# Kernel tuning notes

Measured on AMD Instinct MI355X. Metric: run time of the kernel, lower is better.

The kernel has to match this reference:

```python
import jax, jax.numpy as jnp
import numpy as np

B, S, D, H = 2, 2048, 1024, 16
HD = D // H  # head_dim = 64


def setup_inputs() -> dict:
    key = jax.random.key(0)
    ks = jax.random.split(key, 5)
    scale = 1.0 / np.sqrt(D)  # xavier-ish init scale
    return {
        "x": jax.random.normal(ks[0], (B, S, D), jnp.float32),
        "Wq": jax.random.normal(ks[1], (D, D), jnp.float32) * scale,
        "Wk": jax.random.normal(ks[2], (D, D), jnp.float32) * scale,
        "Wv": jax.random.normal(ks[3], (D, D), jnp.float32) * scale,
        "Wo": jax.random.normal(ks[4], (D, D), jnp.float32) * scale,
        "bo": jnp.zeros((D,), jnp.float32),
    }


def reference(x, Wq, Wk, Wv, Wo, bo):
    # nn.Linear stores weight as [out, in]; y = x @ W.T
    b, s, d = x.shape
    def heads(t):
        return t.reshape(b, s, H, HD).transpose(0, 2, 1, 3)  # [B,H,S,HD]
    Q = heads(x @ Wq.T)
    K = heads(x @ Wk.T)
    V = heads(x @ Wv.T)
    # Chunked loop in the original sees all K per Q-chunk => full attention.
    scores = jnp.einsum("bhqd,bhkd->bhqk", Q, K) / np.sqrt(HD)
    attn = jax.nn.softmax(scores, axis=-1)
    out = jnp.einsum("bhqk,bhkd->bhqd", attn, V)
    out = out.transpose(0, 2, 1, 3).reshape(b, s, d)
    return out @ Wo.T + bo
```

## Files before the change

### kernel.cpp

```cpp
#include <hip/hip_runtime.h>
#include <hip/hip_bf16.h>
#include <math.h>

#define Bc 2
#define Sc 2048
#define Dc 1024
#define Hc 16
#define HDc 64
#define Mc (Bc*Sc)

using f32x4  = __attribute__((ext_vector_type(4))) float;
using bf16x8 = __attribute__((ext_vector_type(8))) short;
using s16x4  = __attribute__((ext_vector_type(4))) short;
using uint4v = __attribute__((ext_vector_type(4))) unsigned int;

#define GAS(p) ((const __attribute__((address_space(1))) void*)(p))
#define LAS(p) ((__attribute__((address_space(3))) void*)(p))

#define QSC 0.18033688011112042f

__device__ __forceinline__ short f2b(float f) {
  union { float f; unsigned u; } v; v.f = f;
  unsigned r = (v.u + 0x7fffu + ((v.u >> 16) & 1u)) >> 16;
  return (short)r;
}

__global__ __launch_bounds__(256) void cvt_all(
    const float* __restrict__ x,
    const float* __restrict__ Wq, const float* __restrict__ Wk,
    const float* __restrict__ Wv, const float* __restrict__ Wo,
    short* __restrict__ xb, short* __restrict__ wqb, short* __restrict__ wkb,
    short* __restrict__ wvb, short* __restrict__ wob) {
  int i = blockIdx.x * 256 + threadIdx.x;
  const float* in; short* out; int idx;
  if (i < (1 << 20)) {
    in = x; out = xb; idx = i;
  } else {
    int j = i - (1 << 20);
    int s = j >> 18; idx = j & 262143;
    in  = (s == 0) ? Wq  : (s == 1) ? Wk  : (s == 2) ? Wv  : Wo;
    out = (s == 0) ? wqb : (s == 1) ? wkb : (s == 2) ? wvb : wob;
  }
  float4 v = reinterpret_cast<const float4*>(in)[idx];
  s16x4 o;
  o.x = f2b(v.x); o.y = f2b(v.y); o.z = f2b(v.z); o.w = f2b(v.w);
  reinterpret_cast<s16x4*>(out)[idx] = o;
}

__device__ __forceinline__ void gemm_core_128(
    const short* __restrict__ A, const short* __restrict__ Bt,
    int m0, int n0, short* As, short* Bs, f32x4 (&acc)[4][4]) {
  const int tid = threadIdx.x;
  const int l = tid & 63;
  const int w = tid >> 6;
  const int wr = w >> 1, wc = w & 1;
  const int g = l >> 4;

  int srow[4], scol[4];
#pragma unroll
  for (int i = 0; i < 4; ++i) {
    int off = w * 1024 + i * 4096 + l * 16;
    int row = off >> 7;
    srow[i] = row;
    scol[i] = (off & 127) ^ ((row & 7) << 4);
  }
  const int rA = (wr * 64 + (l & 15)) * 128;
  const int rB = (wc * 64 + (l & 15)) * 128;
  const int sw = (l & 7) << 4;

  for (int kt = 0; kt < 16; ++kt) {
#pragma unroll
    for (int i = 0; i < 4; ++i) {
      const char* ga = (const char*)A + (size_t)(m0 + srow[i]) * 2048 + kt * 128 + scol[i];
      const char* gb = (const char*)Bt + (size_t)(n0 + srow[i]) * 2048 + kt * 128 + scol[i];
      __builtin_amdgcn_global_load_lds(GAS(ga), LAS((char*)As + w * 1024 + i * 4096), 16, 0, 0);
      __builtin_amdgcn_global_load_lds(GAS(gb), LAS((char*)Bs + w * 1024 + i * 4096), 16, 0, 0);
    }
    __syncthreads();
#pragma unroll
    for (int ks = 0; ks < 2; ++ks) {
      bf16x8 af[4], bfr[4];
#pragma unroll
      for (int mi = 0; mi < 4; ++mi)
        af[mi] = *(const bf16x8*)((const char*)As + rA + mi * 2048 + ((g * 16 + ks * 64) ^ sw));
#pragma unroll
      for (int ni = 0; ni < 4; ++ni)
        bfr[ni] = *(const bf16x8*)((const char*)Bs + rB + ni * 2048 + ((g * 16 + ks * 64) ^ sw));
#pragma unroll
      for (int mi = 0; mi < 4; ++mi)
#pragma unroll
        for (int ni = 0; ni < 4; ++ni)
          acc[mi][ni] = __builtin_amdgcn_mfma_f32_16x16x32_bf16(af[mi], bfr[ni], acc[mi][ni], 0, 0, 0);
    }
    __syncthreads();
  }
}

__global__ __launch_bounds__(256) void qkv_kernel(
    const short* __restrict__ xb, const short* __restrict__ wq,
    const short* __restrict__ wk, const short* __restrict__ wv,
    short* __restrict__ Qb, short* __restrict__ Kb, short* __restrict__ Vtg) {
  __shared__ short As[128 * 64];
  __shared__ short Bs[128 * 64];
  const int mt = blockIdx.x, yb = blockIdx.y;
  const int sel = yb >> 3, nb = yb & 7;
  const short* Wt = (sel == 0) ? wq : (sel == 1) ? wk : wv;
  f32x4 acc[4][4];
#pragma unroll
  for (int i = 0; i < 4; ++i)
#pragma unroll
    for (int j = 0; j < 4; ++j)
#pragma unroll
      for (int r = 0; r < 4; ++r) acc[i][j][r] = 0.0f;
  gemm_core_128(xb, Wt, mt * 128, nb * 128, As, Bs, acc);
  const int l = threadIdx.x & 63, w = threadIdx.x >> 6;
  const int wr = w >> 1, wc = w & 1, g = l >> 4, c = l & 15;

  if (sel == 2) {
#pragma unroll
    for (int mi = 0; mi < 4; ++mi)
#pragma unroll
      for (int ni = 0; ni < 4; ++ni) {
        int n = nb * 128 + wc * 64 + ni * 16 + c;
        int h = n >> 6, hd = n & 63;
        int m = mt * 128 + wr * 64 + mi * 16 + g * 4;
        int b = m >> 11, s = m & 2047;
        s16x4 pk;
#pragma unroll
        for (int r = 0; r < 4; ++r) pk[r] = f2b(acc[mi][ni][r]);
        *(s16x4*)(Vtg + ((size_t)(b * 16 + h) * 64 + hd) * 2048 + s) = pk;
      }
  } else {
    short* Ob = (sel == 0) ? Qb : Kb;
    const float oscale = (sel == 0) ? QSC : 1.0f;
#pragma unroll
    for (int mi = 0; mi < 4; ++mi)
#pragma unroll
      for (int ni = 0; ni < 4; ++ni) {
        int n = nb * 128 + wc * 64 + ni * 16 + c;
        int h = n >> 6, hd = n & 63;
#pragma unroll
        for (int r = 0; r < 4; ++r) {
          int m = mt * 128 + wr * 64 + mi * 16 + g * 4 + r;
          int b = m >> 11, s = m & 2047;
          Ob[((size_t)(b * 16 + h) * 2048 + s) * 64 + hd] = f2b(acc[mi][ni][r] * oscale);
        }
      }
  }
}

__global__ __launch_bounds__(256) void oproj_kernel(
    const short* __restrict__ ab, const short* __restrict__ wo,
    const float* __restrict__ bo, float* __restrict__ out) {
  __shared__ short As[128 * 64];
  __shared__ short Bs[128 * 64];
  const int mt = blockIdx.x, nb = blockIdx.y;
  f32x4 acc[4][4];
#pragma unroll
  for (int i = 0; i < 4; ++i)
#pragma unroll
    for (int j = 0; j < 4; ++j)
#pragma unroll
      for (int r = 0; r < 4; ++r) acc[i][j][r] = 0.0f;
  gemm_core_128(ab, wo, mt * 128, nb * 128, As, Bs, acc);
  const int l = threadIdx.x & 63, w = threadIdx.x >> 6;
  const int wr = w >> 1, wc = w & 1, g = l >> 4;
#pragma unroll
  for (int mi = 0; mi < 4; ++mi)
#pragma unroll
    for (int ni = 0; ni < 4; ++ni) {
      int n = nb * 128 + wc * 64 + ni * 16 + (l & 15);
      float bias = bo[n];
#pragma unroll
      for (int r = 0; r < 4; ++r) {
        int m = mt * 128 + wr * 64 + mi * 16 + g * 4 + r;
        out[(size_t)m * 1024 + n] = acc[mi][ni][r] + bias;
      }
    }
}

__global__ __launch_bounds__(512, 4) void attn_kernel(
    const short* __restrict__ Qb, const short* __restrict__ Kb,
    const short* __restrict__ Vtg, short* __restrict__ ab) {
  __shared__ char lds[49152];
  const int bh = blockIdx.x;
  const int qt = blockIdx.y;
  const int tid = threadIdx.x, l = tid & 63, w = tid >> 6;
  const int qg = w >> 1, h = w & 1;
  const int g = l >> 4, c = l & 15;
  const int sw = (l & 7) << 4;
  const bool godd = (l & 16) != 0;
  const short* Qp = Qb + (size_t)bh * Sc * HDc;
  const char* KpB = (const char*)(Kb + (size_t)bh * Sc * HDc);
  const char* VtB = (const char*)(Vtg + (size_t)bh * Sc * HDc);
  const int q0 = qt * 128 + qg * 32;

  bf16x8 bq[2][2];
#pragma unroll
  for (int qf = 0; qf < 2; ++qf)
#pragma unroll
    for (int ks = 0; ks < 2; ++ks)
      bq[qf][ks] = *(const bf16x8*)(Qp + (size_t)(q0 + qf * 16 + c) * 64 + ks * 32 + g * 8);

  f32x4 o[2][4];
  float lsum[2] = {0.0f, 0.0f};
#pragma unroll
  for (int qf = 0; qf < 2; ++qf)
#pragma unroll
    for (int ohf = 0; ohf < 4; ++ohf)
#pragma unroll
      for (int r = 0; r < 4; ++r) o[qf][ohf][r] = 0.0f;

  const int soff = w * 1024 + l * 16;
  const int srow = soff >> 7;
  const int scol = (soff & 127) ^ ((srow & 7) << 4);
  const size_t koff = (size_t)srow * 128 + scol;
  const size_t voff = (size_t)srow * 4096 + scol;
  const int ldst = w * 1024;

#define ISSUE3(t_) do {                                                               \
    char* kd_ = lds + ((t_) % 3) * 8192 + ldst;                                       \
    char* vd_ = lds + 24576 + ((t_) % 3) * 8192 + ldst;                               \
    __builtin_amdgcn_global_load_lds(GAS(KpB + (size_t)(t_) * 8192 + koff), LAS(kd_), 16, 0, 0); \
    __builtin_amdgcn_global_load_lds(GAS(VtB + (size_t)(t_) * 128  + voff), LAS(vd_), 16, 0, 0); \
  } while (0)

  ISSUE3(0);
  ISSUE3(1);

  for (int t = 0; t < 32; ++t) {
    if (t < 31) {
      asm volatile("s_waitcnt vmcnt(2)" ::: "memory");
    } else {
      asm volatile("s_waitcnt vmcnt(0)" ::: "memory");
    }
    __builtin_amdgcn_s_barrier();
    if (t < 30) ISSUE3(t + 2);

    const char* KsB = lds + (t % 3) * 8192;
    const char* VsB = lds + 24576 + (t % 3) * 8192;

    f32x4 s[2][2];
#pragma unroll
    for (int qf = 0; qf < 2; ++qf)
#pragma unroll
      for (int kf2 = 0; kf2 < 2; ++kf2)
#pragma unroll
        for (int r = 0; r < 4; ++r) s[qf][kf2][r] = 0.0f;
#pragma unroll
    for (int ks = 0; ks < 2; ++ks) {
      bf16x8 ak[2];
#pragma unroll
      for (int kf2 = 0; kf2 < 2; ++kf2) {
        int row = (2 * h + kf2) * 16 + c;
        ak[kf2] = *(const bf16x8*)(KsB + row * 128 + ((ks * 64 + g * 16) ^ sw));
      }
      __builtin_amdgcn_s_setprio(1);
#pragma unroll
      for (int qf = 0; qf < 2; ++qf)
#pragma unroll
        for (int kf2 = 0; kf2 < 2; ++kf2)
          s[qf][kf2] = __builtin_amdgcn_mfma_f32_16x16x32_bf16(ak[kf2], bq[qf][ks], s[qf][kf2], 0, 0, 0);
      __builtin_amdgcn_s_setprio(0);
    }

    bf16x8 pb[2];
#pragma unroll
    for (int qf = 0; qf < 2; ++qf) {
      float p[2][4];
#pragma unroll
      for (int kf2 = 0; kf2 < 2; ++kf2)
#pragma unroll
        for (int r = 0; r < 4; ++r)
          p[kf2][r] = __builtin_amdgcn_exp2f(s[qf][kf2][r]);
      float t0 = (p[0][0] + p[0][1]) + (p[0][2] + p[0][3]);
      float t1 = (p[1][0] + p[1][1]) + (p[1][2] + p[1][3]);
      lsum[qf] += t0 + t1;

      unsigned dw[2][2];
#pragma unroll
      for (int kf2 = 0; kf2 < 2; ++kf2)
#pragma unroll
        for (int d = 0; d < 2; ++d)
          asm("v_cvt_pk_bf16_f32 %0, %1, %2" : "=v"(dw[kf2][d]) : "v"(p[kf2][2 * d]), "v"(p[kf2][2 * d + 1]));

      unsigned T[4];
#pragma unroll
      for (int d = 0; d < 2; ++d) {
        unsigned Av = dw[0][d], Bv = dw[1][d];
        asm("v_permlane32_swap_b32 %0, %1" : "+v"(Av), "+v"(Bv));
        unsigned sAv = (unsigned)__shfl_xor((int)Av, 16);
        unsigned sBv = (unsigned)__shfl_xor((int)Bv, 16);
        T[d]     = godd ? sBv : Av;
        T[d + 2] = godd ? Bv  : sAv;
      }
      uint4v t4; t4.x = T[0]; t4.y = T[1]; t4.z = T[2]; t4.w = T[3];
      pb[qf] = __builtin_bit_cast(bf16x8, t4);
    }

    {
      bf16x8 av[4];
#pragma unroll
      for (int ohf = 0; ohf < 4; ++ohf) {
        int row = ohf * 16 + c;
        av[ohf] = *(const bf16x8*)(VsB + row * 128 + ((h * 64 + g * 16) ^ sw));
      }
      __builtin_amdgcn_s_setprio(1);
#pragma unroll
      for (int ohf = 0; ohf < 4; ++ohf) {
        o[0][ohf] = __builtin_amdgcn_mfma_f32_16x16x32_bf16(av[ohf], pb[0], o[0][ohf], 0, 0, 0);
        o[1][ohf] = __builtin_amdgcn_mfma_f32_16x16x32_bf16(av[ohf], pb[1], o[1][ohf], 0, 0, 0);
      }
      __builtin_amdgcn_s_setprio(0);
    }
  }

  float* So = (float*)lds;
  float* Sl = (float*)(lds + 24576);
  const int b = bh >> 4, hh = bh & 15;
  float lv[2];

  __syncthreads();
#pragma unroll
  for (int qf = 0; qf < 2; ++qf) {
    if (h == 1) {
#pragma unroll
      for (int ohf = 0; ohf < 4; ++ohf)
        *(f32x4*)(So + qg * 1024 + l * 16 + ohf * 4) = o[qf][ohf];
      if (qf == 0) {
        Sl[qg * 128 + l * 2 + 0] = lsum[0];
        Sl[qg * 128 + l * 2 + 1] = lsum[1];
      }
    }
    __syncthreads();
    if (h == 0) {
      if (qf == 0) {
#pragma unroll
        for (int j = 0; j < 2; ++j) {
          float lt = lsum[j] + Sl[qg * 128 + l * 2 + j];
          lt += __shfl_xor(lt, 16);
          lt += __shfl_xor(lt, 32);
          lv[j] = 1.0f / lt;
        }
      }
      int q = q0 + qf * 16 + c;
      short* dst = ab + (size_t)(b * Sc + q) * Dc + hh * 64 + g * 4;
#pragma unroll
      for (int ohf = 0; ohf < 4; ++ohf) {
        f32x4 om = o[qf][ohf] + *(const f32x4*)(So + qg * 1024 + l * 16 + ohf * 4);
        s16x4 pk4;
#pragma unroll
        for (int r = 0; r < 4; ++r) pk4[r] = f2b(om[r] * lv[qf]);
        *(s16x4*)(dst + ohf * 16) = pk4;
      }
    }
    __syncthreads();
  }
}

extern "C" void kernel_launch(void* const* d_in, const int* in_sizes, int n_in,
                              void* d_out, int out_size, void* d_ws, size_t ws_size,
                              hipStream_t stream) {
  const float* x  = (const float*)d_in[0];
  const float* Wq = (const float*)d_in[1];
  const float* Wk = (const float*)d_in[2];
  const float* Wv = (const float*)d_in[3];
  const float* Wo = (const float*)d_in[4];
  const float* bo = (const float*)d_in[5];
  float* out = (float*)d_out;

  char* p = (char*)d_ws;
  short* xb    = (short*)p; p += (size_t)Mc * Dc * 2;
  short* wqb   = (short*)p; p += (size_t)Dc * Dc * 2;
  short* wkb   = (short*)p; p += (size_t)Dc * Dc * 2;
  short* wvb   = (short*)p; p += (size_t)Dc * Dc * 2;
  short* wob   = (short*)p; p += (size_t)Dc * Dc * 2;
  short* Qb    = (short*)p; p += (size_t)Mc * Dc * 2;
  short* Kb    = (short*)p; p += (size_t)Mc * Dc * 2;
  short* Vtg   = (short*)p; p += (size_t)Mc * Dc * 2;
  short* attnb = (short*)p; p += (size_t)Mc * Dc * 2;

  cvt_all<<<8192, 256, 0, stream>>>(x, Wq, Wk, Wv, Wo, xb, wqb, wkb, wvb, wob);
  qkv_kernel<<<dim3(Mc / 128, 24), 256, 0, stream>>>(xb, wqb, wkb, wvb, Qb, Kb, Vtg);
  attn_kernel<<<dim3(Bc * Hc, Sc / 128), 512, 0, stream>>>(Qb, Kb, Vtg, attnb);
  oproj_kernel<<<dim3(Mc / 128, Dc / 128), 256, 0, stream>>>(attnb, wob, bo, out);
}
```

Measured before the change: 192.1 us.

## Halve attention query tile to 64 rows to double grid and raise occupancy

```diff
diff --git a/kernel.cpp b/kernel.cpp
--- a/kernel.cpp
+++ b/kernel.cpp
@@ -179,7 +179,7 @@
     }
 }
 
-__global__ __launch_bounds__(512, 4) void attn_kernel(
+__global__ __launch_bounds__(512, 6) void attn_kernel(
     const short* __restrict__ Qb, const short* __restrict__ Kb,
     const short* __restrict__ Vtg, short* __restrict__ ab) {
   __shared__ char lds[49152];
@@ -193,23 +193,19 @@
   const short* Qp = Qb + (size_t)bh * Sc * HDc;
   const char* KpB = (const char*)(Kb + (size_t)bh * Sc * HDc);
   const char* VtB = (const char*)(Vtg + (size_t)bh * Sc * HDc);
-  const int q0 = qt * 128 + qg * 32;
-
-  bf16x8 bq[2][2];
-#pragma unroll
-  for (int qf = 0; qf < 2; ++qf)
-#pragma unroll
-    for (int ks = 0; ks < 2; ++ks)
-      bq[qf][ks] = *(const bf16x8*)(Qp + (size_t)(q0 + qf * 16 + c) * 64 + ks * 32 + g * 8);
-
-  f32x4 o[2][4];
-  float lsum[2] = {0.0f, 0.0f};
-#pragma unroll
-  for (int qf = 0; qf < 2; ++qf)
-#pragma unroll
-    for (int ohf = 0; ohf < 4; ++ohf)
-#pragma unroll
-      for (int r = 0; r < 4; ++r) o[qf][ohf][r] = 0.0f;
+  const int q0 = qt * 64 + qg * 16;
+
+  bf16x8 bq[2];
+#pragma unroll
+  for (int ks = 0; ks < 2; ++ks)
+    bq[ks] = *(const bf16x8*)(Qp + (size_t)(q0 + c) * 64 + ks * 32 + g * 8);
+
+  f32x4 o[4];
+  float lsum = 0.0f;
+#pragma unroll
+  for (int ohf = 0; ohf < 4; ++ohf)
+#pragma unroll
+    for (int r = 0; r < 4; ++r) o[ohf][r] = 0.0f;
 
   const int soff = w * 1024 + l * 16;
   const int srow = soff >> 7;
@@ -240,13 +236,11 @@
     const char* KsB = lds + (t % 3) * 8192;
     const char* VsB = lds + 24576 + (t % 3) * 8192;
 
-    f32x4 s[2][2];
-#pragma unroll
-    for (int qf = 0; qf < 2; ++qf)
-#pragma unroll
-      for (int kf2 = 0; kf2 < 2; ++kf2)
-#pragma unroll
-        for (int r = 0; r < 4; ++r) s[qf][kf2][r] = 0.0f;
+    f32x4 s[2];
+#pragma unroll
+    for (int kf2 = 0; kf2 < 2; ++kf2)
+#pragma unroll
+      for (int r = 0; r < 4; ++r) s[kf2][r] = 0.0f;
 #pragma unroll
     for (int ks = 0; ks < 2; ++ks) {
       bf16x8 ak[2];
@@ -257,25 +251,22 @@
       }
       __builtin_amdgcn_s_setprio(1);
 #pragma unroll
-      for (int qf = 0; qf < 2; ++qf)
-#pragma unroll
-        for (int kf2 = 0; kf2 < 2; ++kf2)
-          s[qf][kf2] = __builtin_amdgcn_mfma_f32_16x16x32_bf16(ak[kf2], bq[qf][ks], s[qf][kf2], 0, 0, 0);
+      for (int kf2 = 0; kf2 < 2; ++kf2)
+        s[kf2] = __builtin_amdgcn_mfma_f32_16x16x32_bf16(ak[kf2], bq[ks], s[kf2], 0, 0, 0);
       __builtin_amdgcn_s_setprio(0);
     }
 
-    bf16x8 pb[2];
-#pragma unroll
-    for (int qf = 0; qf < 2; ++qf) {
+    bf16x8 pb;
+    {
       float p[2][4];
 #pragma unroll
       for (int kf2 = 0; kf2 < 2; ++kf2)
 #pragma unroll
         for (int r = 0; r < 4; ++r)
-          p[kf2][r] = __builtin_amdgcn_exp2f(s[qf][kf2][r]);
+          p[kf2][r] = __builtin_amdgcn_exp2f(s[kf2][r]);
       float t0 = (p[0][0] + p[0][1]) + (p[0][2] + p[0][3]);
       float t1 = (p[1][0] + p[1][1]) + (p[1][2] + p[1][3]);
-      lsum[qf] += t0 + t1;
+      lsum += t0 + t1;
 
       unsigned dw[2][2];
 #pragma unroll
@@ -295,7 +286,7 @@
         T[d + 2] = godd ? Bv  : sAv;
       }
       uint4v t4; t4.x = T[0]; t4.y = T[1]; t4.z = T[2]; t4.w = T[3];
-      pb[qf] = __builtin_bit_cast(bf16x8, t4);
+      pb = __builtin_bit_cast(bf16x8, t4);
     }
 
     {
@@ -307,54 +298,39 @@
       }
       __builtin_amdgcn_s_setprio(1);
 #pragma unroll
-      for (int ohf = 0; ohf < 4; ++ohf) {
-        o[0][ohf] = __builtin_amdgcn_mfma_f32_16x16x32_bf16(av[ohf], pb[0], o[0][ohf], 0, 0, 0);
-        o[1][ohf] = __builtin_amdgcn_mfma_f32_16x16x32_bf16(av[ohf], pb[1], o[1][ohf], 0, 0, 0);
-      }
+      for (int ohf = 0; ohf < 4; ++ohf)
+        o[ohf] = __builtin_amdgcn_mfma_f32_16x16x32_bf16(av[ohf], pb, o[ohf], 0, 0, 0);
       __builtin_amdgcn_s_setprio(0);
     }
   }
 
-  float* So = (float*)lds;
   float* Sl = (float*)(lds + 24576);
   const int b = bh >> 4, hh = bh & 15;
-  float lv[2];
 
   __syncthreads();
-#pragma unroll
-  for (int qf = 0; qf < 2; ++qf) {
-    if (h == 1) {
-#pragma unroll
-      for (int ohf = 0; ohf < 4; ++ohf)
-        *(f32x4*)(So + qg * 1024 + l * 16 + ohf * 4) = o[qf][ohf];
-      if (qf == 0) {
-        Sl[qg * 128 + l * 2 + 0] = lsum[0];
-        Sl[qg * 128 + l * 2 + 1] = lsum[1];
-      }
-    }
-    __syncthreads();
-    if (h == 0) {
-      if (qf == 0) {
-#pragma unroll
-        for (int j = 0; j < 2; ++j) {
-          float lt = lsum[j] + Sl[qg * 128 + l * 2 + j];
-          lt += __shfl_xor(lt, 16);
-          lt += __shfl_xor(lt, 32);
-          lv[j] = 1.0f / lt;
-        }
-      }
-      int q = q0 + qf * 16 + c;
-      short* dst = ab + (size_t)(b * Sc + q) * Dc + hh * 64 + g * 4;
-#pragma unroll
-      for (int ohf = 0; ohf < 4; ++ohf) {
-        f32x4 om = o[qf][ohf] + *(const f32x4*)(So + qg * 1024 + l * 16 + ohf * 4);
-        s16x4 pk4;
-#pragma unroll
-        for (int r = 0; r < 4; ++r) pk4[r] = f2b(om[r] * lv[qf]);
-        *(s16x4*)(dst + ohf * 16) = pk4;
-      }
-    }
-    __syncthreads();
+  if (h == 1) {
+#pragma unroll
+    for (int ohf = 0; ohf < 4; ++ohf)
+      *(f32x4*)(lds + qg * 4096 + ((l * 64 + ohf * 16) ^ ((l & 7) << 4))) = o[ohf];
+    Sl[qg * 64 + l] = lsum;
+  }
+  __syncthreads();
+  if (h == 0) {
+    float lt = lsum + Sl[qg * 64 + l];
+    lt += __shfl_xor(lt, 16);
+    lt += __shfl_xor(lt, 32);
+    float inv = 1.0f / lt;
+    int q = q0 + c;
+    short* dst = ab + (size_t)(b * Sc + q) * Dc + hh * 64 + g * 4;
+#pragma unroll
+    for (int ohf = 0; ohf < 4; ++ohf) {
+      f32x4 om = o[ohf] +
+          *(const f32x4*)(lds + qg * 4096 + ((l * 64 + ohf * 16) ^ ((l & 7) << 4)));
+      s16x4 pk4;
+#pragma unroll
+      for (int r = 0; r < 4; ++r) pk4[r] = f2b(om[r] * inv);
+      *(s16x4*)(dst + ohf * 16) = pk4;
+    }
   }
 }
 
@@ -382,6 +358,6 @@
 
   cvt_all<<<8192, 256, 0, stream>>>(x, Wq, Wk, Wv, Wo, xb, wqb, wkb, wvb, wob);
   qkv_kernel<<<dim3(Mc / 128, 24), 256, 0, stream>>>(xb, wqb, wkb, wvb, Qb, Kb, Vtg);
-  attn_kernel<<<dim3(Bc * Hc, Sc / 128), 512, 0, stream>>>(Qb, Kb, Vtg, attnb);
+  attn_kernel<<<dim3(Bc * Hc, Sc / 64), 512, 0, stream>>>(Qb, Kb, Vtg, attnb);
   oproj_kernel<<<dim3(Mc / 128, Dc / 128), 256, 0, stream>>>(attnb, wob, bo, out);
 }
```

Result: slower. 201.5 us (+4.9%).

## Rewrite QKV GEMM as 256x256 tile with pipelined async LDS loads

Applied to the files above, without the earlier changes.

```diff
diff --git a/kernel.cpp b/kernel.cpp
--- a/kernel.cpp
+++ b/kernel.cpp
@@ -18,6 +18,9 @@
 #define LAS(p) ((__attribute__((address_space(3))) void*)(p))
 
 #define QSC 0.18033688011112042f
+
+#define SCB __builtin_amdgcn_sched_barrier(0)
+#define BARR __builtin_amdgcn_s_barrier()
 
 __device__ __forceinline__ short f2b(float f) {
   union { float f; unsigned u; } v; v.f = f;
@@ -96,34 +99,137 @@
   }
 }
 
-__global__ __launch_bounds__(256) void qkv_kernel(
+__global__ __launch_bounds__(512, 2) void qkv_kernel(
     const short* __restrict__ xb, const short* __restrict__ wq,
     const short* __restrict__ wk, const short* __restrict__ wv,
     short* __restrict__ Qb, short* __restrict__ Kb, short* __restrict__ Vtg) {
-  __shared__ short As[128 * 64];
-  __shared__ short Bs[128 * 64];
-  const int mt = blockIdx.x, yb = blockIdx.y;
-  const int sel = yb >> 3, nb = yb & 7;
+  __shared__ char lds[131072];
+  const int tid = threadIdx.x, l = tid & 63, w = tid >> 6;
+  const int g = l >> 4, c = l & 15;
+  const int sw = (l & 7) << 4;
+  const int wm = w >> 2, wn = w & 3;
+  const int mt = blockIdx.x, nb = blockIdx.y;
+  const int sel = nb >> 2, nbq = nb & 3;
   const short* Wt = (sel == 0) ? wq : (sel == 1) ? wk : wv;
-  f32x4 acc[4][4];
-#pragma unroll
-  for (int i = 0; i < 4; ++i)
+  const char* Ag = (const char*)xb;
+  const char* Bg = (const char*)Wt;
+
+  const int la = (w & 3) * 64 + l;
+  const int lb = (w >> 2) * 64 + l;
+  const int arow0 = la >> 3;
+  const int acol  = ((la * 16) & 127) ^ ((arow0 & 7) << 4);
+  const int brow0 = lb >> 3;
+  const int bcol  = ((lb * 16) & 127) ^ ((brow0 & 7) << 4);
+
+#define STG_A(t_, hi_) do {                                                           \
+    char* d_ = lds + ((((t_) & 1) * 2 + wm) << 14) + (w & 3) * 1024 + (hi_) * 8192;   \
+    const char* s_ = Ag + (size_t)(mt * 256 + wm * 128 + (hi_) * 64 + arow0) * 2048   \
+                     + (t_) * 128 + acol;                                             \
+    __builtin_amdgcn_global_load_lds(GAS(s_), LAS(d_), 16, 0, 0);                     \
+    __builtin_amdgcn_global_load_lds(GAS(s_ + 32 * 2048), LAS(d_ + 4096), 16, 0, 0);  \
+  } while (0)
+
+#define STG_B(t_, hi_) do {                                                           \
+    char* d_ = lds + 65536 + ((t_) & 1) * 32768 + wn * 8192 + (w >> 2) * 1024         \
+               + (hi_) * 4096;                                                        \
+    const char* s_ = Bg + (size_t)(nbq * 256 + wn * 64 + (hi_) * 32 + brow0) * 2048   \
+                     + (t_) * 128 + bcol;                                             \
+    __builtin_amdgcn_global_load_lds(GAS(s_), LAS(d_), 16, 0, 0);                     \
+    __builtin_amdgcn_global_load_lds(GAS(s_ + 16 * 2048), LAS(d_ + 2048), 16, 0, 0);  \
+  } while (0)
+
+  f32x4 acc[8][4];
+#pragma unroll
+  for (int i = 0; i < 8; ++i)
 #pragma unroll
     for (int j = 0; j < 4; ++j)
 #pragma unroll
       for (int r = 0; r < 4; ++r) acc[i][j][r] = 0.0f;
-  gemm_core_128(xb, Wt, mt * 128, nb * 128, As, Bs, acc);
-  const int l = threadIdx.x & 63, w = threadIdx.x >> 6;
-  const int wr = w >> 1, wc = w & 1, g = l >> 4, c = l & 15;
+
+  bf16x8 a[4][2], blo[2][2], bhi[2][2];
+
+#define LD_A(mh_) do {                                                                \
+    _Pragma("unroll")                                                                 \
+    for (int mi2 = 0; mi2 < 4; ++mi2)                                                 \
+      _Pragma("unroll")                                                               \
+      for (int ks = 0; ks < 2; ++ks)                                                  \
+        a[mi2][ks] = *(const bf16x8*)(Ah + ((mh_) * 64 + mi2 * 16 + c) * 128 +        \
+                                      ((ks * 64 + g * 16) ^ sw));                     \
+  } while (0)
+
+#define LD_B(arr_, nh_) do {                                                          \
+    _Pragma("unroll")                                                                 \
+    for (int ni2 = 0; ni2 < 2; ++ni2)                                                 \
+      _Pragma("unroll")                                                               \
+      for (int ks = 0; ks < 2; ++ks)                                                  \
+        arr_[ni2][ks] = *(const bf16x8*)(Bq + ((nh_) * 32 + ni2 * 16 + c) * 128 +     \
+                                         ((ks * 64 + g * 16) ^ sw));                  \
+  } while (0)
+
+#define MMQ(mh_, arr_, nh_) do {                                                      \
+    __builtin_amdgcn_s_setprio(1);                                                    \
+    _Pragma("unroll")                                                                 \
+    for (int ks = 0; ks < 2; ++ks)                                                    \
+      _Pragma("unroll")                                                               \
+      for (int mi2 = 0; mi2 < 4; ++mi2)                                               \
+        _Pragma("unroll")                                                             \
+        for (int ni2 = 0; ni2 < 2; ++ni2)                                             \
+          acc[(mh_) * 4 + mi2][(nh_) * 2 + ni2] =                                     \
+              __builtin_amdgcn_mfma_f32_16x16x32_bf16(                                \
+                  a[mi2][ks], arr_[ni2][ks], acc[(mh_) * 4 + mi2][(nh_) * 2 + ni2],   \
+                  0, 0, 0);                                                           \
+    __builtin_amdgcn_s_setprio(0);                                                    \
+  } while (0)
+
+  STG_A(0, 0); STG_B(0, 0); STG_B(0, 1); STG_A(0, 1);
+  asm volatile("s_waitcnt vmcnt(4)" ::: "memory");
+  BARR; SCB;
+
+  for (int t = 0; t < 16; ++t) {
+    const int db = t & 1;
+    const char* Ah = lds + ((db * 2 + wm) << 14);
+    const char* Bq = lds + 65536 + db * 32768 + wn * 8192;
+    const bool st = t < 15;
+
+    LD_A(0); LD_B(blo, 0);
+    if (st) STG_A(t + 1, 0);
+    BARR; SCB;
+    MMQ(0, blo, 0);
+    if (st) asm volatile("s_waitcnt vmcnt(4)" ::: "memory");
+    else    asm volatile("s_waitcnt vmcnt(2)" ::: "memory");
+    BARR; SCB;
+
+    LD_B(bhi, 1);
+    if (st) STG_B(t + 1, 0);
+    BARR; SCB;
+    MMQ(0, bhi, 1);
+    if (st) asm volatile("s_waitcnt vmcnt(4)" ::: "memory");
+    else    asm volatile("s_waitcnt vmcnt(0)" ::: "memory");
+    BARR; SCB;
+
+    LD_A(1);
+    if (st) STG_B(t + 1, 1);
+    BARR; SCB;
+    MMQ(1, bhi, 1);
+    BARR; SCB;
+
+    if (st) STG_A(t + 1, 1);
+    BARR; SCB;
+    MMQ(1, blo, 0);
+    if (st) {
+      asm volatile("s_waitcnt vmcnt(4)" ::: "memory");
+      BARR; SCB;
+    }
+  }
 
   if (sel == 2) {
 #pragma unroll
-    for (int mi = 0; mi < 4; ++mi)
+    for (int mi = 0; mi < 8; ++mi)
 #pragma unroll
       for (int ni = 0; ni < 4; ++ni) {
-        int n = nb * 128 + wc * 64 + ni * 16 + c;
+        int n = nbq * 256 + wn * 64 + ni * 16 + c;
         int h = n >> 6, hd = n & 63;
-        int m = mt * 128 + wr * 64 + mi * 16 + g * 4;
+        int m = mt * 256 + wm * 128 + mi * 16 + g * 4;
         int b = m >> 11, s = m & 2047;
         s16x4 pk;
 #pragma unroll
@@ -134,14 +240,14 @@
     short* Ob = (sel == 0) ? Qb : Kb;
     const float oscale = (sel == 0) ? QSC : 1.0f;
 #pragma unroll
-    for (int mi = 0; mi < 4; ++mi)
+    for (int mi = 0; mi < 8; ++mi)
 #pragma unroll
       for (int ni = 0; ni < 4; ++ni) {
-        int n = nb * 128 + wc * 64 + ni * 16 + c;
+        int n = nbq * 256 + wn * 64 + ni * 16 + c;
         int h = n >> 6, hd = n & 63;
 #pragma unroll
         for (int r = 0; r < 4; ++r) {
-          int m = mt * 128 + wr * 64 + mi * 16 + g * 4 + r;
+          int m = mt * 256 + wm * 128 + mi * 16 + g * 4 + r;
           int b = m >> 11, s = m & 2047;
           Ob[((size_t)(b * 16 + h) * 2048 + s) * 64 + hd] = f2b(acc[mi][ni][r] * oscale);
         }
@@ -315,7 +421,6 @@
     }
   }
 
-  float* So = (float*)lds;
   float* Sl = (float*)(lds + 24576);
   const int b = bh >> 4, hh = bh & 15;
   float lv[2];
@@ -326,7 +431,7 @@
     if (h == 1) {
 #pragma unroll
       for (int ohf = 0; ohf < 4; ++ohf)
-        *(f32x4*)(So + qg * 1024 + l * 16 + ohf * 4) = o[qf][ohf];
+        *(f32x4*)(lds + qg * 4096 + ((l * 64 + ohf * 16) ^ ((l & 7) << 4))) = o[qf][ohf];
       if (qf == 0) {
         Sl[qg * 128 + l * 2 + 0] = lsum[0];
         Sl[qg * 128 + l * 2 + 1] = lsum[1];
@@ -347,7 +452,8 @@
       short* dst = ab + (size_t)(b * Sc + q) * Dc + hh * 64 + g * 4;
 #pragma unroll
       for (int ohf = 0; ohf < 4; ++ohf) {
-        f32x4 om = o[qf][ohf] + *(const f32x4*)(So + qg * 1024 + l * 16 + ohf * 4);
+        f32x4 om = o[qf][ohf] +
+            *(const f32x4*)(lds + qg * 4096 + ((l * 64 + ohf * 16) ^ ((l & 7) << 4)));
         s16x4 pk4;
 #pragma unroll
         for (int r = 0; r < 4; ++r) pk4[r] = f2b(om[r] * lv[qf]);
@@ -381,7 +487,7 @@
   short* attnb = (short*)p; p += (size_t)Mc * Dc * 2;
 
   cvt_all<<<8192, 256, 0, stream>>>(x, Wq, Wk, Wv, Wo, xb, wqb, wkb, wvb, wob);
-  qkv_kernel<<<dim3(Mc / 128, 24), 256, 0, stream>>>(xb, wqb, wkb, wvb, Qb, Kb, Vtg);
+  qkv_kernel<<<dim3(Mc / 256, 12), 512, 0, stream>>>(xb, wqb, wkb, wvb, Qb, Kb, Vtg);
   attn_kernel<<<dim3(Bc * Hc, Sc / 128), 512, 0, stream>>>(Qb, Kb, Vtg, attnb);
   oproj_kernel<<<dim3(Mc / 128, Dc / 128), 256, 0, stream>>>(attnb, wob, bo, out);
 }
```

New measurement: 187.2 us. 1.03x faster.
